# Performance work log

Hardware: AMD Instinct MI355X
Metric: run time of the kernel (lower is better)

## Reference

```python
import jax, jax.numpy as jnp
import numpy as np

DIM = 256
SCALE = DIM ** -0.5  # head_dim == dim since num_heads == 1


def setup_inputs() -> dict:
    key = jax.random.key(0)
    ks = jax.random.split(key, 8)
    B, NQ, NK = 8, 2048, 4096
    q = jax.random.normal(ks[0], (B, NQ, DIM), dtype=jnp.float32)
    k = jax.random.normal(ks[1], (B, NK, DIM), dtype=jnp.float32)
    v = jax.random.normal(ks[2], (B, NK, DIM), dtype=jnp.float32)
    supp_mask = jax.random.randint(ks[3], (B, NK), 0, 2) == 1  # bool [B, NK]
    s = 1.0 / np.sqrt(DIM)
    Wq = jax.random.normal(ks[4], (DIM, DIM), dtype=jnp.float32) * s
    Wk = jax.random.normal(ks[5], (DIM, DIM), dtype=jnp.float32) * s
    Wv = jax.random.normal(ks[6], (DIM, DIM), dtype=jnp.float32) * s
    Wp = jax.random.normal(ks[7], (DIM, DIM), dtype=jnp.float32) * s
    return {"q": q, "k": k, "v": v, "supp_mask": supp_mask,
            "Wq": Wq, "Wk": Wk, "Wv": Wv, "Wp": Wp}


def reference(q, k, v, supp_mask, Wq, Wk, Wv, Wp):
    # Linear layers (torch: x @ W.T, no bias)
    qh = q @ Wq.T                      # [B, NQ, D]
    kh = k @ Wk.T                      # [B, NK, D]
    vh = v @ Wv.T                      # [B, NK, D]
    attn = jnp.einsum('bqd,bkd->bqk', qh, kh) * SCALE  # [B, NQ, NK]
    # additive mask: (~mask) * -10000, broadcast over queries
    add = jnp.where(supp_mask, 0.0, -10000.0)[:, None, :]
    attn = jax.nn.softmax(attn + add, axis=-1)
    x = jnp.einsum('bqk,bkd->bqd', attn, vh)           # [B, NQ, D]
    return x @ Wp.T
```

## Files before the change

kernel.cpp:

```cpp
#include <hip/hip_runtime.h>
#include <hip/hip_bf16.h>

typedef __bf16 bf16x8 __attribute__((ext_vector_type(8)));
typedef __bf16 bf16x4v __attribute__((ext_vector_type(4)));
typedef float f32x4 __attribute__((ext_vector_type(4)));
typedef float f32x16 __attribute__((ext_vector_type(16)));
typedef unsigned int u32;
typedef u32 u32x4 __attribute__((ext_vector_type(4)));
typedef unsigned short u16;

#define MFMA16(a, b, c) __builtin_amdgcn_mfma_f32_16x16x32_bf16((a), (b), (c), 0, 0, 0)
#define MFMA32(a, b, c) __builtin_amdgcn_mfma_f32_32x32x16_bf16((a), (b), (c), 0, 0, 0)

static constexpr float QSCALE = 0.09016844f;
static constexpr float MADD   = -14427.0f;

__device__ inline u32 pk2(float a, float b) {
    u16 x = __builtin_bit_cast(u16, (__bf16)a);
    u16 y = __builtin_bit_cast(u16, (__bf16)b);
    return (u32)x | ((u32)y << 16);
}

__device__ inline void gl16(const void* g, void* l) {
    __builtin_amdgcn_global_load_lds((const __attribute__((address_space(1))) u32*)g,
                                     (__attribute__((address_space(3))) u32*)l, 16, 0, 0);
}

template<bool IN_F32, bool OUT_F32, bool TRANS_OUT>
__global__ __launch_bounds__(256, 3)
void proj_kernel(const void* __restrict__ Xv, const float* __restrict__ W,
                 void* __restrict__ Yv, float oscale)
{
    __shared__ __bf16 lds_a[64][72];
    __shared__ __bf16 lds_b[256][72];
    const int t = threadIdx.x;
    const int row0 = blockIdx.x * 64;
    const int lane = t & 63, w = t >> 6;
    const int wr = w >> 1, wc = w & 1;
    const int lr = lane & 15, lg = lane >> 4;

    f32x4 acc[2][8] = {};

    for (int kk = 0; kk < 4; ++kk) {
        __syncthreads();
        if constexpr (IN_F32) {
            const float* X = (const float*)Xv;
            #pragma unroll
            for (int p = 0; p < 4; ++p) {
                int idx4 = p * 256 + t;
                int r = idx4 >> 4, c4 = (idx4 & 15) << 2;
                float4 v4 = *(const float4*)&X[(size_t)(row0 + r) * 256 + kk * 64 + c4];
                bf16x4v pk = { (__bf16)v4.x, (__bf16)v4.y, (__bf16)v4.z, (__bf16)v4.w };
                *(bf16x4v*)&lds_a[r][c4] = pk;
            }
        } else {
            const __bf16* X = (const __bf16*)Xv;
            #pragma unroll
            for (int p = 0; p < 2; ++p) {
                int idx8 = p * 256 + t;
                int r = idx8 >> 3, c8 = (idx8 & 7) << 3;
                *(bf16x8*)&lds_a[r][c8] = *(const bf16x8*)&X[(size_t)(row0 + r) * 256 + kk * 64 + c8];
            }
        }
        #pragma unroll
        for (int p = 0; p < 16; ++p) {
            int idx4 = p * 256 + t;
            int r = idx4 >> 4, c4 = (idx4 & 15) << 2;
            float4 v4 = *(const float4*)&W[(size_t)r * 256 + kk * 64 + c4];
            bf16x4v pk = { (__bf16)v4.x, (__bf16)v4.y, (__bf16)v4.z, (__bf16)v4.w };
            *(bf16x4v*)&lds_b[r][c4] = pk;
        }
        __syncthreads();
        #pragma unroll
        for (int ks = 0; ks < 2; ++ks) {
            bf16x8 af[2], bfr[8];
            #pragma unroll
            for (int i = 0; i < 2; ++i)
                af[i] = *(bf16x8*)&lds_a[wr * 32 + i * 16 + lr][ks * 32 + 8 * lg];
            #pragma unroll
            for (int j = 0; j < 8; ++j)
                bfr[j] = *(bf16x8*)&lds_b[wc * 128 + j * 16 + lr][ks * 32 + 8 * lg];
            #pragma unroll
            for (int i = 0; i < 2; ++i)
                #pragma unroll
                for (int j = 0; j < 8; ++j)
                    acc[i][j] = MFMA16(af[i], bfr[j], acc[i][j]);
        }
    }

    if constexpr (TRANS_OUT) {
        __bf16* Y = (__bf16*)Yv;
        #pragma unroll
        for (int i = 0; i < 2; ++i) {
            int mbase = row0 + wr * 32 + i * 16 + 4 * lg;
            int bb = mbase >> 12, mm = mbase & 4095;
            #pragma unroll
            for (int j = 0; j < 8; ++j) {
                int n = wc * 128 + j * 16 + lr;
                bf16x4v pk = { (__bf16)acc[i][j][0], (__bf16)acc[i][j][1],
                               (__bf16)acc[i][j][2], (__bf16)acc[i][j][3] };
                *(bf16x4v*)&Y[(((size_t)bb * 256 + n) << 12) + mm] = pk;
            }
        }
    } else if constexpr (OUT_F32) {
        float* Y = (float*)Yv;
        #pragma unroll
        for (int i = 0; i < 2; ++i)
            #pragma unroll
            for (int j = 0; j < 8; ++j) {
                int n = wc * 128 + j * 16 + lr;
                #pragma unroll
                for (int r = 0; r < 4; ++r) {
                    int m = row0 + wr * 32 + i * 16 + 4 * lg + r;
                    Y[(size_t)m * 256 + n] = acc[i][j][r];
                }
            }
    } else {
        __bf16* Y = (__bf16*)Yv;
        #pragma unroll
        for (int i = 0; i < 2; ++i)
            #pragma unroll
            for (int j = 0; j < 8; ++j) {
                int n = wc * 128 + j * 16 + lr;
                #pragma unroll
                for (int r = 0; r < 4; ++r) {
                    int m = row0 + wr * 32 + i * 16 + 4 * lg + r;
                    Y[(size_t)m * 256 + n] = (__bf16)(acc[i][j][r] * oscale);
                }
            }
    }
}

__global__ __launch_bounds__(256, 2)
void attn_kernel(const __bf16* __restrict__ qh, const __bf16* __restrict__ kh,
                 const __bf16* __restrict__ vt, const int* __restrict__ mask,
                 __bf16* __restrict__ part, float* __restrict__ ml)
{
    extern __shared__ char smem[];

    const int t = threadIdx.x, lane = t & 63, w = t >> 6;
    const int col = lane & 31, hi = lane >> 5;
    const int bid = blockIdx.x;
    const int b = bid & 7, rest = bid >> 3;
    const int split = rest & 3, qb = rest >> 2;
    const int q0 = qb * 128;
    const int kbase = split * 1024;

    bf16x8 qf[16];
    {
        const size_t qrow = (size_t)b * 2048 + q0 + w * 32 + col;
        #pragma unroll
        for (int s = 0; s < 16; ++s)
            qf[s] = *(const bf16x8*)&qh[qrow * 256 + s * 16 + 8 * hi];
    }

    int koff[4];
    #pragma unroll
    for (int i = 0; i < 4; ++i) {
        int rrel = i * 2 + hi;
        koff[i] = rrel * 512 + ((col ^ rrel) << 4);
    }
    const int voffl = ((lane >> 2) << 13) + (((lane & 3) ^ ((lane >> 3) & 3)) << 4);

    const char* kp = (const char*)(kh + ((size_t)b * 4096 + kbase + w * 8) * 256);
    const char* vp = (const char*)(vt + ((size_t)(b * 256 + w * 64)) * 4096 + kbase);

    auto stage = [&](int kt, int buf) {
        const char* ks = kp + (size_t)kt * 16384;
        const char* vs = vp + (size_t)kt * 64;
        char* kd = smem + buf * 32768 + w * 4096;
        char* vd = smem + buf * 32768 + 16384 + w * 4096;
        #pragma unroll
        for (int i = 0; i < 4; ++i) gl16(ks + koff[i], kd + i * 1024);
        #pragma unroll
        for (int i = 0; i < 4; ++i) gl16(vs + voffl + i * 131072, vd + i * 1024);
    };

    f32x16 o[8] = {};
    float m_run = -3.0e38f, lsum = 0.0f;
    const u32x4 onesf = { hi ? 0u : 0x00003F80u, 0u, 0u, 0u };

    int mv = mask[b * 4096 + kbase + col];
    stage(0, 0);
    __syncthreads();
    int cur = 0;

    for (int kt = 0; kt < 32; ++kt) {
        int mvn = 0;
        if (kt + 1 < 32) {
            stage(kt + 1, cur ^ 1);
            mvn = mask[b * 4096 + kbase + (kt + 1) * 32 + col];
        }
        const char* lk = smem + cur * 32768;
        const char* lv = smem + cur * 32768 + 16384;

        float mh = mv ? 0.0f : MADD;
        u32x4 mf = { hi ? 0u : pk2(mh, 0.0f), 0u, 0u, 0u };
        f32x16 st = {};
        st = MFMA32(__builtin_bit_cast(bf16x8, mf), __builtin_bit_cast(bf16x8, onesf), st);

        __builtin_amdgcn_s_setprio(1);
        #pragma unroll
        for (int s = 0; s < 16; ++s) {
            bf16x8 ka = *(const bf16x8*)(lk + col * 512 + (((2 * s + hi) ^ (col & 7)) << 4));
            st = MFMA32(ka, qf[s], st);
        }
        __builtin_amdgcn_s_setprio(0);

        float pmax = st[0];
        #pragma unroll
        for (int r = 1; r < 16; ++r) pmax = fmaxf(pmax, st[r]);
        pmax = fmaxf(pmax, __shfl_xor(pmax, 32));
        if (__any(pmax > m_run + 8.0f)) {
            float mnew = fmaxf(m_run, pmax);
            float alpha = exp2f(m_run - mnew);
            m_run = mnew;
            lsum *= alpha;
            #pragma unroll
            for (int r = 0; r < 16; ++r) {
                float a = __shfl(alpha, (r & 3) + 8 * (r >> 2) + 4 * hi);
                #pragma unroll
                for (int dt = 0; dt < 8; ++dt) o[dt][r] *= a;
            }
        }
        #pragma unroll
        for (int r = 0; r < 16; ++r) { st[r] = exp2f(st[r] - m_run); lsum += st[r]; }

        __builtin_amdgcn_s_setprio(1);
        #pragma unroll
        for (int c = 0; c < 2; ++c) {
            u32 a0 = pk2(st[8 * c + 0], st[8 * c + 1]);
            u32 a1 = pk2(st[8 * c + 2], st[8 * c + 3]);
            u32 b0 = pk2(st[8 * c + 4], st[8 * c + 5]);
            u32 b1 = pk2(st[8 * c + 6], st[8 * c + 7]);
            u32 a0s = __shfl_xor((int)a0, 32), a1s = __shfl_xor((int)a1, 32);
            u32 b0s = __shfl_xor((int)b0, 32), b1s = __shfl_xor((int)b1, 32);
            u32x4 pa;
            pa[0] = hi ? b0s : a0;  pa[1] = hi ? b1s : a1;
            pa[2] = hi ? b0  : a0s; pa[3] = hi ? b1  : a1s;
            bf16x8 paf = __builtin_bit_cast(bf16x8, pa);
            #pragma unroll
            for (int dt = 0; dt < 8; ++dt) {
                bf16x8 vb = *(const bf16x8*)(lv + (dt * 32 + col) * 64 +
                                             ((((c << 1) | hi) ^ ((col >> 1) & 3)) << 4));
                o[dt] = MFMA32(paf, vb, o[dt]);
            }
        }
        __builtin_amdgcn_s_setprio(0);

        mv = mvn;
        __syncthreads();
        cur ^= 1;
    }

    lsum += __shfl_xor(lsum, 32);
    if (lane < 32) {
        size_t qa = (size_t)b * 2048 + q0 + w * 32 + lane;
        ml[((size_t)split * 16384 + qa) * 2]     = m_run;
        ml[((size_t)split * 16384 + qa) * 2 + 1] = lsum;
    }
    float inv = 1.0f / lsum;
    #pragma unroll
    for (int r = 0; r < 16; ++r) {
        int ql = (r & 3) + 8 * (r >> 2) + 4 * hi;
        float ir = __shfl(inv, ql);
        size_t base = ((size_t)split * 16384 + (size_t)b * 2048 + q0 + w * 32 + ql) * 256;
        #pragma unroll
        for (int dt = 0; dt < 8; ++dt)
            part[base + dt * 32 + col] = (__bf16)(o[dt][r] * ir);
    }
}

__global__ __launch_bounds__(256, 8)
void combine_kernel(const __bf16* __restrict__ part, const float* __restrict__ ml,
                    __bf16* __restrict__ xh)
{
    int tid = blockIdx.x * 256 + threadIdx.x;
    int row = tid >> 5, d8 = (tid & 31) * 8;
    float mm[4], ll[4];
    #pragma unroll
    for (int s = 0; s < 4; ++s) {
        mm[s] = ml[((size_t)s * 16384 + row) * 2];
        ll[s] = ml[((size_t)s * 16384 + row) * 2 + 1];
    }
    float ms = fmaxf(fmaxf(mm[0], mm[1]), fmaxf(mm[2], mm[3]));
    float ws[4], L = 0.0f;
    #pragma unroll
    for (int s = 0; s < 4; ++s) { ws[s] = ll[s] * exp2f(mm[s] - ms); L += ws[s]; }
    float acc[8] = {};
    #pragma unroll
    for (int s = 0; s < 4; ++s) {
        bf16x8 v = *(const bf16x8*)&part[((size_t)s * 16384 + row) * 256 + d8];
        #pragma unroll
        for (int j = 0; j < 8; ++j) acc[j] += ws[s] * (float)v[j];
    }
    float invL = 1.0f / L;
    bf16x8 o8;
    #pragma unroll
    for (int j = 0; j < 8; ++j) o8[j] = (__bf16)(acc[j] * invL);
    *(bf16x8*)&xh[(size_t)row * 256 + d8] = o8;
}

extern "C" void kernel_launch(void* const* d_in, const int* in_sizes, int n_in,
                              void* d_out, int out_size, void* d_ws, size_t ws_size,
                              hipStream_t stream)
{
    (void)in_sizes; (void)n_in; (void)out_size; (void)ws_size;
    const float* q  = (const float*)d_in[0];
    const float* k  = (const float*)d_in[1];
    const float* v  = (const float*)d_in[2];
    const int* mask = (const int*)d_in[3];
    const float* Wq = (const float*)d_in[4];
    const float* Wk = (const float*)d_in[5];
    const float* Wv = (const float*)d_in[6];
    const float* Wp = (const float*)d_in[7];
    float* out = (float*)d_out;

    __bf16* qh = (__bf16*)d_ws;
    __bf16* kh = qh + (size_t)16384 * 256;
    __bf16* vt = kh + (size_t)32768 * 256;
    __bf16* xh = vt + (size_t)32768 * 256;

    __bf16* part = (__bf16*)d_in[1];
    float*  mlp  = (float*)d_in[0];

    proj_kernel<true,  false, false><<<256, 256, 0, stream>>>(q, Wq, qh, QSCALE);
    proj_kernel<true,  false, false><<<512, 256, 0, stream>>>(k, Wk, kh, 1.0f);
    proj_kernel<true,  false, true ><<<512, 256, 0, stream>>>(v, Wv, vt, 1.0f);

    hipFuncSetAttribute((const void*)attn_kernel,
                        hipFuncAttributeMaxDynamicSharedMemorySize, 65536);
    attn_kernel<<<512, 256, 65536, stream>>>(qh, kh, vt, mask, part, mlp);
    combine_kernel<<<2048, 256, 0, stream>>>(part, mlp, xh);

    proj_kernel<false, true,  false><<<256, 256, 0, stream>>>(xh, Wp, out, 1.0f);
}
```

Before: 331.5 us.

## Pre-convert weights to swizzled bf16 and enlarge attention tiles to 64 keys

Adds a kernel that converts all four weight matrices to bf16 once, in a swizzled layout. The projection kernels now stage those weights straight into LDS with async global-to-LDS loads instead of converting fp32 on every block. The attention kernel moves to 512-thread blocks covering 256 queries, and each step processes 64 keys using two score accumulators with 128KB of LDS. This halves the number of loop iterations and barriers and improves K/V reuse per block, at the cost of more registers, an occupancy of one block per CU, and writing xh into an input buffer.

```diff
diff --git a/kernel.cpp b/kernel.cpp
--- a/kernel.cpp
+++ b/kernel.cpp
@@ -26,13 +26,32 @@
                                      (__attribute__((address_space(3))) u32*)l, 16, 0, 0);
 }
 
+__global__ __launch_bounds__(256, 8)
+void wcvt_kernel(const float* __restrict__ Wq, const float* __restrict__ Wk,
+                 const float* __restrict__ Wv, const float* __restrict__ Wp,
+                 __bf16* __restrict__ wbf)
+{
+    const int bid = blockIdx.x;
+    const int widx = bid >> 5;
+    const float* W = widx == 0 ? Wq : widx == 1 ? Wk : widx == 2 ? Wv : Wp;
+    const int tid = (bid & 31) * 256 + threadIdx.x;
+    const int n = tid >> 5, g = tid & 31;
+    const int sg = (g & ~7) | ((g & 7) ^ (n & 7));
+    const float* src = W + n * 256 + sg * 8;
+    float4 a = *(const float4*)src;
+    float4 b = *(const float4*)(src + 4);
+    bf16x8 o8 = { (__bf16)a.x, (__bf16)a.y, (__bf16)a.z, (__bf16)a.w,
+                  (__bf16)b.x, (__bf16)b.y, (__bf16)b.z, (__bf16)b.w };
+    *(bf16x8*)&wbf[(size_t)widx * 65536 + n * 256 + g * 8] = o8;
+}
+
 template<bool IN_F32, bool OUT_F32, bool TRANS_OUT>
-__global__ __launch_bounds__(256, 3)
-void proj_kernel(const void* __restrict__ Xv, const float* __restrict__ W,
+__global__ __launch_bounds__(256, 2)
+void proj_kernel(const void* __restrict__ Xv, const __bf16* __restrict__ wbf,
                  void* __restrict__ Yv, float oscale)
 {
     __shared__ __bf16 lds_a[64][72];
-    __shared__ __bf16 lds_b[256][72];
+    __shared__ __bf16 lds_w[256][64];
     const int t = threadIdx.x;
     const int row0 = blockIdx.x * 64;
     const int lane = t & 63, w = t >> 6;
@@ -43,6 +62,21 @@
 
     for (int kk = 0; kk < 4; ++kk) {
         __syncthreads();
+        {
+            char* lw = (char*)&lds_w[0][0];
+            const char* src = (const char*)(wbf + kk * 64);
+            #pragma unroll
+            for (int i = 0; i < 2; ++i) {
+                int r = i * 32 + w * 8 + (lane >> 3);
+                (void)r;
+            }
+            #pragma unroll
+            for (int i = 0; i < 8; ++i) {
+                int r = i * 32 + w * 8 + (lane >> 3);
+                gl16(src + (size_t)r * 512 + (lane & 7) * 16,
+                     lw + i * 4096 + w * 1024 + (lane & 63) * 16);
+            }
+        }
         if constexpr (IN_F32) {
             const float* X = (const float*)Xv;
             #pragma unroll
@@ -62,14 +96,6 @@
                 *(bf16x8*)&lds_a[r][c8] = *(const bf16x8*)&X[(size_t)(row0 + r) * 256 + kk * 64 + c8];
             }
         }
-        #pragma unroll
-        for (int p = 0; p < 16; ++p) {
-            int idx4 = p * 256 + t;
-            int r = idx4 >> 4, c4 = (idx4 & 15) << 2;
-            float4 v4 = *(const float4*)&W[(size_t)r * 256 + kk * 64 + c4];
-            bf16x4v pk = { (__bf16)v4.x, (__bf16)v4.y, (__bf16)v4.z, (__bf16)v4.w };
-            *(bf16x4v*)&lds_b[r][c4] = pk;
-        }
         __syncthreads();
         #pragma unroll
         for (int ks = 0; ks < 2; ++ks) {
@@ -78,8 +104,11 @@
             for (int i = 0; i < 2; ++i)
                 af[i] = *(bf16x8*)&lds_a[wr * 32 + i * 16 + lr][ks * 32 + 8 * lg];
             #pragma unroll
-            for (int j = 0; j < 8; ++j)
-                bfr[j] = *(bf16x8*)&lds_b[wc * 128 + j * 16 + lr][ks * 32 + 8 * lg];
+            for (int j = 0; j < 8; ++j) {
+                int rw = wc * 128 + j * 16 + lr;
+                int ch = (ks * 4 + lg) ^ (rw & 7);
+                bfr[j] = *(bf16x8*)((char*)&lds_w[0][0] + rw * 128 + ch * 16);
+            }
             #pragma unroll
             for (int i = 0; i < 2; ++i)
                 #pragma unroll
@@ -131,7 +160,7 @@
     }
 }
 
-__global__ __launch_bounds__(256, 2)
+__global__ __launch_bounds__(512, 1)
 void attn_kernel(const __bf16* __restrict__ qh, const __bf16* __restrict__ kh,
                  const __bf16* __restrict__ vt, const int* __restrict__ mask,
                  __bf16* __restrict__ part, float* __restrict__ ml)
@@ -143,7 +172,7 @@
     const int bid = blockIdx.x;
     const int b = bid & 7, rest = bid >> 3;
     const int split = rest & 3, qb = rest >> 2;
-    const int q0 = qb * 128;
+    const int q0 = qb * 256;
     const int kbase = split * 1024;
 
     bf16x8 qf[16];
@@ -160,56 +189,64 @@
         int rrel = i * 2 + hi;
         koff[i] = rrel * 512 + ((col ^ rrel) << 4);
     }
-    const int voffl = ((lane >> 2) << 13) + (((lane & 3) ^ ((lane >> 3) & 3)) << 4);
+    const int voffl = ((lane >> 3) << 13) + (((lane & 7) ^ ((lane >> 3) & 7)) << 4);
 
     const char* kp = (const char*)(kh + ((size_t)b * 4096 + kbase + w * 8) * 256);
-    const char* vp = (const char*)(vt + ((size_t)(b * 256 + w * 64)) * 4096 + kbase);
+    const char* vp = (const char*)(vt + ((size_t)(b * 256 + w * 32)) * 4096 + kbase);
 
     auto stage = [&](int kt, int buf) {
-        const char* ks = kp + (size_t)kt * 16384;
-        const char* vs = vp + (size_t)kt * 64;
-        char* kd = smem + buf * 32768 + w * 4096;
-        char* vd = smem + buf * 32768 + 16384 + w * 4096;
-        #pragma unroll
-        for (int i = 0; i < 4; ++i) gl16(ks + koff[i], kd + i * 1024);
-        #pragma unroll
-        for (int i = 0; i < 4; ++i) gl16(vs + voffl + i * 131072, vd + i * 1024);
+        const char* ks = kp + (size_t)kt * 32768;
+        const char* vs = vp + (size_t)kt * 128;
+        char* kd = smem + buf * 65536 + w * 4096;
+        char* vd = smem + buf * 65536 + 32768 + w * 4096;
+        #pragma unroll
+        for (int i = 0; i < 4; ++i) gl16(ks + koff[i], kd + i * 1024 + lane * 16);
+        #pragma unroll
+        for (int i = 0; i < 4; ++i) gl16(vs + voffl + i * 65536, vd + i * 1024 + (lane & 63) * 16);
     };
 
     f32x16 o[8] = {};
     float m_run = -3.0e38f, lsum = 0.0f;
     const u32x4 onesf = { hi ? 0u : 0x00003F80u, 0u, 0u, 0u };
 
-    int mv = mask[b * 4096 + kbase + col];
+    int mv = mask[b * 4096 + kbase + lane];
     stage(0, 0);
     __syncthreads();
     int cur = 0;
 
-    for (int kt = 0; kt < 32; ++kt) {
+    for (int kt = 0; kt < 16; ++kt) {
         int mvn = 0;
-        if (kt + 1 < 32) {
+        if (kt + 1 < 16) {
             stage(kt + 1, cur ^ 1);
-            mvn = mask[b * 4096 + kbase + (kt + 1) * 32 + col];
-        }
-        const char* lk = smem + cur * 32768;
-        const char* lv = smem + cur * 32768 + 16384;
+            mvn = mask[b * 4096 + kbase + (kt + 1) * 64 + lane];
+        }
+        const char* lk = smem + cur * 65536;
+        const char* lv = smem + cur * 65536 + 32768;
 
         float mh = mv ? 0.0f : MADD;
-        u32x4 mf = { hi ? 0u : pk2(mh, 0.0f), 0u, 0u, 0u };
-        f32x16 st = {};
-        st = MFMA32(__builtin_bit_cast(bf16x8, mf), __builtin_bit_cast(bf16x8, onesf), st);
+        float mo = __shfl_xor(mh, 32);
+        u32x4 mf0 = { hi ? 0u : pk2(mh, 0.0f), 0u, 0u, 0u };
+        u32x4 mf1 = { hi ? 0u : pk2(mo, 0.0f), 0u, 0u, 0u };
+        f32x16 st0 = {}, st1 = {};
+        st0 = MFMA32(__builtin_bit_cast(bf16x8, mf0), __builtin_bit_cast(bf16x8, onesf), st0);
+        st1 = MFMA32(__builtin_bit_cast(bf16x8, mf1), __builtin_bit_cast(bf16x8, onesf), st1);
 
         __builtin_amdgcn_s_setprio(1);
         #pragma unroll
         for (int s = 0; s < 16; ++s) {
-            bf16x8 ka = *(const bf16x8*)(lk + col * 512 + (((2 * s + hi) ^ (col & 7)) << 4));
-            st = MFMA32(ka, qf[s], st);
+            int ch = ((2 * s + hi) ^ (col & 7)) << 4;
+            bf16x8 ka0 = *(const bf16x8*)(lk + col * 512 + ch);
+            bf16x8 ka1 = *(const bf16x8*)(lk + (col + 32) * 512 + ch);
+            st0 = MFMA32(ka0, qf[s], st0);
+            st1 = MFMA32(ka1, qf[s], st1);
         }
         __builtin_amdgcn_s_setprio(0);
 
-        float pmax = st[0];
-        #pragma unroll
-        for (int r = 1; r < 16; ++r) pmax = fmaxf(pmax, st[r]);
+        float pmax = st0[0];
+        #pragma unroll
+        for (int r = 1; r < 16; ++r) pmax = fmaxf(pmax, st0[r]);
+        #pragma unroll
+        for (int r = 0; r < 16; ++r) pmax = fmaxf(pmax, st1[r]);
         pmax = fmaxf(pmax, __shfl_xor(pmax, 32));
         if (__any(pmax > m_run + 8.0f)) {
             float mnew = fmaxf(m_run, pmax);
@@ -224,15 +261,28 @@
             }
         }
         #pragma unroll
-        for (int r = 0; r < 16; ++r) { st[r] = exp2f(st[r] - m_run); lsum += st[r]; }
+        for (int r = 0; r < 16; ++r) st0[r] = exp2f(st0[r] - m_run);
+        #pragma unroll
+        for (int r = 0; r < 16; ++r) st1[r] = exp2f(st1[r] - m_run);
+        {
+            float s0 = 0, s1 = 0, s2 = 0, s3 = 0;
+            #pragma unroll
+            for (int r = 0; r < 4; ++r) {
+                s0 += st0[r] + st0[r + 4]; s1 += st0[r + 8] + st0[r + 12];
+                s2 += st1[r] + st1[r + 4]; s3 += st1[r + 8] + st1[r + 12];
+            }
+            lsum += (s0 + s1) + (s2 + s3);
+        }
 
         __builtin_amdgcn_s_setprio(1);
         #pragma unroll
-        for (int c = 0; c < 2; ++c) {
-            u32 a0 = pk2(st[8 * c + 0], st[8 * c + 1]);
-            u32 a1 = pk2(st[8 * c + 2], st[8 * c + 3]);
-            u32 b0 = pk2(st[8 * c + 4], st[8 * c + 5]);
-            u32 b1 = pk2(st[8 * c + 6], st[8 * c + 7]);
+        for (int c = 0; c < 4; ++c) {
+            const f32x16& pp = (c < 2) ? st0 : st1;
+            int rb = (c & 1) * 8;
+            u32 a0 = pk2(pp[rb + 0], pp[rb + 1]);
+            u32 a1 = pk2(pp[rb + 2], pp[rb + 3]);
+            u32 b0 = pk2(pp[rb + 4], pp[rb + 5]);
+            u32 b1 = pk2(pp[rb + 6], pp[rb + 7]);
             u32 a0s = __shfl_xor((int)a0, 32), a1s = __shfl_xor((int)a1, 32);
             u32 b0s = __shfl_xor((int)b0, 32), b1s = __shfl_xor((int)b1, 32);
             u32x4 pa;
@@ -241,8 +291,8 @@
             bf16x8 paf = __builtin_bit_cast(bf16x8, pa);
             #pragma unroll
             for (int dt = 0; dt < 8; ++dt) {
-                bf16x8 vb = *(const bf16x8*)(lv + (dt * 32 + col) * 64 +
-                                             ((((c << 1) | hi) ^ ((col >> 1) & 3)) << 4));
+                bf16x8 vb = *(const bf16x8*)(lv + (dt * 32 + col) * 128 +
+                                             ((((c << 1) | hi) ^ (col & 7)) << 4));
                 o[dt] = MFMA32(paf, vb, o[dt]);
             }
         }
@@ -316,22 +366,25 @@
     const float* Wp = (const float*)d_in[7];
     float* out = (float*)d_out;
 
-    __bf16* qh = (__bf16*)d_ws;
-    __bf16* kh = qh + (size_t)16384 * 256;
-    __bf16* vt = kh + (size_t)32768 * 256;
-    __bf16* xh = vt + (size_t)32768 * 256;
+    __bf16* qh  = (__bf16*)d_ws;
+    __bf16* kh  = qh + (size_t)16384 * 256;
+    __bf16* vt  = kh + (size_t)32768 * 256;
+    __bf16* wbf = vt + (size_t)32768 * 256;
 
     __bf16* part = (__bf16*)d_in[1];
     float*  mlp  = (float*)d_in[0];
-
-    proj_kernel<true,  false, false><<<256, 256, 0, stream>>>(q, Wq, qh, QSCALE);
-    proj_kernel<true,  false, false><<<512, 256, 0, stream>>>(k, Wk, kh, 1.0f);
-    proj_kernel<true,  false, true ><<<512, 256, 0, stream>>>(v, Wv, vt, 1.0f);
+    __bf16* xh   = (__bf16*)d_in[2];
+
+    wcvt_kernel<<<128, 256, 0, stream>>>(Wq, Wk, Wv, Wp, wbf);
+
+    proj_kernel<true,  false, false><<<256, 256, 0, stream>>>(q, wbf,           qh, QSCALE);
+    proj_kernel<true,  false, false><<<512, 256, 0, stream>>>(k, wbf + 65536,   kh, 1.0f);
+    proj_kernel<true,  false, true ><<<512, 256, 0, stream>>>(v, wbf + 131072,  vt, 1.0f);
 
     hipFuncSetAttribute((const void*)attn_kernel,
-                        hipFuncAttributeMaxDynamicSharedMemorySize, 65536);
-    attn_kernel<<<512, 256, 65536, stream>>>(qh, kh, vt, mask, part, mlp);
+                        hipFuncAttributeMaxDynamicSharedMemorySize, 131072);
+    attn_kernel<<<256, 512, 131072, stream>>>(qh, kh, vt, mask, part, mlp);
     combine_kernel<<<2048, 256, 0, stream>>>(part, mlp, xh);
 
-    proj_kernel<false, true,  false><<<256, 256, 0, stream>>>(xh, Wp, out, 1.0f);
-}
+    proj_kernel<false, true,  false><<<256, 256, 0, stream>>>(xh, wbf + 196608, out, 1.0f);
+}
```

Result: slower. 461.6 us (+39.3%).
